# Optimization experiments

Hardware: AMD Instinct MI355X
Metric: run time of the kernel (lower is better)

Reference implementation:

```python
import jax, jax.numpy as jnp
import numpy as np

# Model config (mirrors init_kwargs)
E = 8          # num_experts
K = 2          # top_k
S = 1          # select_top_k
THRESHOLD = 0.7
NORM_TOPK = True
H = 1024       # hidden_dim
F = 1024       # moe intermediate dim
B, SEQ = 2, 1024


def setup_inputs() -> dict:
    key = jax.random.key(0)
    k1, k2, k3, k4, k5 = jax.random.split(key, 5)
    hidden_states = jax.random.normal(k1, (B, SEQ, H), jnp.float32)
    gate_weight = jax.random.normal(k2, (E, H), jnp.float32) * 0.02
    gate_up_proj = jax.random.normal(k3, (E, 2 * F, H), jnp.float32) * 0.02
    down_proj = jax.random.normal(k4, (E, H, F), jnp.float32) * 0.02
    sim = jax.random.uniform(k5, (E, E), jnp.float32)
    sim = (sim + sim.T) / 2.0
    sim = sim.at[jnp.arange(E), jnp.arange(E)].set(1.0)  # fill_diagonal_(1.0)
    return {
        "hidden_states": hidden_states,
        "gate_weight": gate_weight,
        "gate_up_proj": gate_up_proj,
        "down_proj": down_proj,
        "similarity_matrix": sim,
    }


def reference(hidden_states, gate_weight, gate_up_proj, down_proj, similarity_matrix):
    b, s, h = hidden_states.shape
    x = hidden_states.reshape(-1, h)                     # [N, H]
    N = x.shape[0]

    # Router: logits -> softmax(fp32) -> topk (+ optional norm)
    logits = x @ gate_weight.T                           # [N, E]
    probs = jax.nn.softmax(logits.astype(jnp.float32), axis=-1)
    top_w, top_i = jax.lax.top_k(probs, K)               # [N, K]
    if NORM_TOPK:
        top_w = top_w / jnp.clip(jnp.sum(top_w, -1, keepdims=True), 1e-12)

    # SERE reroute: primary = union of top-S experts over batch; map each
    # secondary expert to its most-similar primary if sim >= threshold.
    primary_mask = jnp.zeros((E,), bool).at[top_i[:, :S].reshape(-1)].set(True)
    sim = jnp.where(primary_mask[None, :], similarity_matrix.astype(jnp.float32), -jnp.inf)
    best_j = jnp.argmax(sim, axis=-1)                    # best primary per expert
    best_sim = jnp.max(sim, axis=-1)
    ids = jnp.arange(E)
    expert_map = jnp.where((~primary_mask) & (best_sim >= THRESHOLD), best_j, ids)
    rerouted = expert_map[top_i]                         # [N, K]

    # Merge duplicate slots via scatter-add, then re-topk K.
    rows = jnp.arange(N)[:, None]
    dense = jnp.zeros((N, E), top_w.dtype).at[rows, rerouted].add(top_w)
    fw, fi = jax.lax.top_k(dense, K)                     # nnz per row <= K, so topk keeps all
    combine = jnp.zeros((N, E), fw.dtype).at[rows, fi].add(jnp.where(fw > 0, fw, 0.0))  # [N, E]

    # Expert MLPs (dense jit-friendly dispatch): silu(gate)*up -> down
    gu = jnp.einsum('nh,efh->enf', x, gate_up_proj)      # [E, N, 2F]
    g, u = jnp.split(gu, 2, axis=-1)
    hmid = jax.nn.silu(g) * u                            # [E, N, F]
    y = jnp.einsum('enf,ehf->enh', hmid, down_proj)      # [E, N, H]
    out = jnp.einsum('ne,enh->nh', combine, y)           # weighted combine
    return out.reshape(b, s, h)
```

## Files before the change

kernel.cpp:

```cpp
#include <hip/hip_runtime.h>
#include <cstdint>
#include <cstddef>

#define N_TOK 2048
#define HID 1024
#define FDIM 1024
#define NE 8
#define PAIR_CAP 5120
#define MT 128
#define BK 64
#define THRESH 0.7f

typedef __attribute__((ext_vector_type(8))) short bf16x8;
typedef __attribute__((ext_vector_type(4))) float f32x4;

static __device__ __forceinline__ unsigned short f2bf(float f) {
  unsigned int u = __float_as_uint(f);
  u += 0x7FFF + ((u >> 16) & 1);
  return (unsigned short)(u >> 16);
}

static __device__ __forceinline__ void gl2lds16(const unsigned short* g, unsigned short* l) {
  __builtin_amdgcn_global_load_lds(
      (const __attribute__((address_space(1))) void*)g,
      (__attribute__((address_space(3))) void*)l, 16, 0, 0);
}

__global__ __launch_bounds__(256) void k_router(
    const float* __restrict__ x, const float* __restrict__ gw,
    unsigned short* __restrict__ xb, float* __restrict__ topw,
    int* __restrict__ topi) {
  __shared__ float sgw[NE * HID];
  int t = threadIdx.x;
#pragma unroll
  for (int i = 0; i < NE * HID / 256; ++i) sgw[t + 256 * i] = gw[t + 256 * i];
  __syncthreads();
  int lane = t & 63;
  int wave = t >> 6;
  int n = blockIdx.x * 4 + wave;
  float acc[NE];
#pragma unroll
  for (int e = 0; e < NE; ++e) acc[e] = 0.f;
#pragma unroll
  for (int i = 0; i < HID / 64; ++i) {
    int h = i * 64 + lane;
    float xv = x[(size_t)n * HID + h];
    xb[(size_t)n * HID + h] = f2bf(xv);
#pragma unroll
    for (int e = 0; e < NE; ++e) acc[e] += xv * sgw[e * HID + h];
  }
#pragma unroll
  for (int off = 32; off > 0; off >>= 1) {
#pragma unroll
    for (int e = 0; e < NE; ++e) acc[e] += __shfl_xor(acc[e], off, 64);
  }
  if (lane == 0) {
    float m = acc[0];
    for (int e = 1; e < NE; ++e) m = fmaxf(m, acc[e]);
    float p[NE]; float s = 0.f;
    for (int e = 0; e < NE; ++e) { p[e] = __expf(acc[e] - m); s += p[e]; }
    float inv = 1.f / s;
    for (int e = 0; e < NE; ++e) p[e] *= inv;
    int i0 = 0; float b0 = p[0];
    for (int e = 1; e < NE; ++e) if (p[e] > b0) { b0 = p[e]; i0 = e; }
    int i1 = -1; float b1 = -1.f;
    for (int e = 0; e < NE; ++e) { if (e == i0) continue; if (p[e] > b1) { b1 = p[e]; i1 = e; } }
    float sw = b0 + b1; if (sw < 1e-12f) sw = 1e-12f;
    topw[n * 2] = b0 / sw; topw[n * 2 + 1] = b1 / sw;
    topi[n * 2] = i0;      topi[n * 2 + 1] = i1;
  }
}

__global__ __launch_bounds__(256) void k_pairs(
    const float* __restrict__ sim, const int* __restrict__ topi,
    const float* __restrict__ topw, int* __restrict__ ctrl,
    int* __restrict__ ptok, float* __restrict__ pw) {
  __shared__ int prim[NE], emap[NE], cnt[NE], soff[NE], cur[NE], padc[NE];
  int t = threadIdx.x;
  if (t < NE) { prim[t] = 0; cnt[t] = 0; }
  __syncthreads();
  for (int n = t; n < N_TOK; n += 256) prim[topi[n * 2]] = 1;
  __syncthreads();
  if (t < NE) {
    float best = -1e30f; int bj = -1;
    for (int j = 0; j < NE; ++j) {
      if (prim[j]) {
        float s = sim[t * NE + j];
        if (s > best) { best = s; bj = j; }
      }
    }
    int m = t;
    if (!prim[t] && bj >= 0 && best >= THRESH) m = bj;
    emap[t] = m;
  }
  __syncthreads();
  for (int n = t; n < N_TOK; n += 256) {
    atomicAdd(&cnt[emap[topi[n * 2]]], 1);
    atomicAdd(&cnt[emap[topi[n * 2 + 1]]], 1);
  }
  __syncthreads();
  if (t == 0) {
    int o = 0;
    for (int e = 0; e < NE; ++e) {
      soff[e] = o;
      int p = (cnt[e] + MT - 1) & ~(MT - 1);
      padc[e] = p; cur[e] = 0; o += p;
    }
  }
  __syncthreads();
  if (t < NE) { ctrl[24 + t] = soff[t]; ctrl[32 + t] = padc[t]; }
  for (int n = t; n < N_TOK; n += 256) {
    int i0 = topi[n * 2], i1 = topi[n * 2 + 1];
    int e0 = emap[i0], e1 = emap[i1];
    int s0 = soff[e0] + atomicAdd(&cur[e0], 1);
    int s1 = soff[e1] + atomicAdd(&cur[e1], 1);
    ptok[s0] = n; pw[s0] = topw[n * 2];
    ptok[s1] = n; pw[s1] = topw[n * 2 + 1];
  }
  __syncthreads();
  for (int e = 0; e < NE; ++e) {
    for (int s = cnt[e] + t; s < padc[e]; s += 256) {
      ptok[soff[e] + s] = 0; pw[soff[e] + s] = 0.f;
    }
  }
}


__global__ __launch_bounds__(256, 2) void k_gemm1(
    const unsigned short* __restrict__ xb, const float* __restrict__ gup,
    unsigned short* __restrict__ hmid, const int* __restrict__ ptok,
    const int* __restrict__ ctrl) {
  int b = blockIdx.x;
  int mt = b >> 8;
  int r8 = b & 255;
  int e = r8 >> 5;
  int y = r8 & 31;
  int padc = ctrl[32 + e];
  if (mt * MT >= padc) return;
  int base = ctrl[24 + e] + mt * MT;
  int f0 = y * 32;

  __shared__ unsigned short As[MT * BK];
  __shared__ unsigned short Bs[64 * BK];
  __shared__ int toks[MT];

  int t = threadIdx.x;
  if (t < MT) toks[t] = ptok[base + t];
  __syncthreads();

  int lane = t & 63;
  int wave = t >> 6;
  int wm = wave >> 1, wn = wave & 1;
  int lm = lane & 15, lh = lane >> 4;

  f32x4 acc[4][2] = {};
  const float* gbase = gup + (size_t)e * 2 * FDIM * HID;

  for (int k0 = 0; k0 < HID; k0 += BK) {
    float4 vb[4];
#pragma unroll
    for (int i = 0; i < 4; ++i) {
      int q = i * 256 + t;
      int r = q >> 4, c4 = q & 15;
      vb[i] = *(const float4*)(gbase + (size_t)(((r >> 4) & 1) * FDIM + f0 + ((r >> 5) << 4) + (r & 15)) * HID + k0 + c4 * 4);
    }
#pragma unroll
    for (int i = 0; i < 4; ++i) {
      int q = i * 256 + t;
      int r = q >> 3;
      int cl = (q & 7) ^ (r & 7);
      gl2lds16(xb + (size_t)toks[r] * HID + k0 + cl * 8, &As[(q & ~63) * 8]);
    }
#pragma unroll
    for (int i = 0; i < 4; ++i) {
      int q = i * 256 + t;
      int r = q >> 4, w = q & 15;
      int pch = (w >> 1) ^ (r & 7);
      unsigned long long pk = (unsigned long long)f2bf(vb[i].x)
          | ((unsigned long long)f2bf(vb[i].y) << 16)
          | ((unsigned long long)f2bf(vb[i].z) << 32)
          | ((unsigned long long)f2bf(vb[i].w) << 48);
      *(unsigned long long*)(&Bs[r * BK + pch * 8 + (w & 1) * 4]) = pk;
    }
    __syncthreads();
#pragma unroll
    for (int kk = 0; kk < 2; ++kk) {
      bf16x8 af[4], bfr[2];
#pragma unroll
      for (int rb = 0; rb < 4; ++rb) {
        int row = wm * 64 + rb * 16 + lm;
        int p = (kk * 4 + lh) ^ (row & 7);
        af[rb] = *(const bf16x8*)(&As[row * BK + p * 8]);
      }
#pragma unroll
      for (int cc = 0; cc < 2; ++cc) {
        int row = wn * 32 + cc * 16 + lm;
        int p = (kk * 4 + lh) ^ (row & 7);
        bfr[cc] = *(const bf16x8*)(&Bs[row * BK + p * 8]);
      }
#pragma unroll
      for (int rb = 0; rb < 4; ++rb) {
#pragma unroll
        for (int cc = 0; cc < 2; ++cc)
          acc[rb][cc] = __builtin_amdgcn_mfma_f32_16x16x32_bf16(af[rb], bfr[cc], acc[rb][cc], 0, 0, 0);
      }
    }
    __syncthreads();
  }
#pragma unroll
  for (int rb = 0; rb < 4; ++rb) {
    int slot = base + wm * 64 + rb * 16 + lh * 4;
    f32x4 g = acc[rb][0];
    f32x4 u = acc[rb][1];
    int f = f0 + wn * 16 + lm;
#pragma unroll
    for (int reg = 0; reg < 4; ++reg) {
      float gv = g[reg];
      float hm = gv / (1.f + __expf(-gv)) * u[reg];
      hmid[(size_t)(slot + reg) * FDIM + f] = f2bf(hm);
    }
  }
}

__global__ __launch_bounds__(256, 2) void k_gemm2(
    const unsigned short* __restrict__ hmid, const float* __restrict__ dwn,
    float* __restrict__ out, const int* __restrict__ ptok,
    const float* __restrict__ pw, const int* __restrict__ ctrl) {
  int b = blockIdx.x;
  int mt = b >> 7;
  int r7 = b & 127;
  int e = r7 >> 4;
  int y = r7 & 15;
  int padc = ctrl[32 + e];
  if (mt * MT >= padc) return;
  int base = ctrl[24 + e] + mt * MT;
  int h0 = y * 64;

  __shared__ unsigned short As[MT * BK];
  __shared__ unsigned short Bs[64 * BK];
  __shared__ int stok[MT];
  __shared__ float spw[MT];

  int t = threadIdx.x;
  if (t < MT) { stok[t] = ptok[base + t]; spw[t] = pw[base + t]; }
  __syncthreads();

  int lane = t & 63;
  int wave = t >> 6;
  int wm = wave >> 1, wn = wave & 1;
  int lm = lane & 15, lh = lane >> 4;

  f32x4 acc[4][2] = {};
  const float* dbase = dwn + (size_t)e * HID * FDIM;

  for (int k0 = 0; k0 < FDIM; k0 += BK) {
    float4 vb[4];
#pragma unroll
    for (int i = 0; i < 4; ++i) {
      int q = i * 256 + t;
      int r = q >> 4, c4 = q & 15;
      vb[i] = *(const float4*)(dbase + (size_t)(h0 + r) * FDIM + k0 + c4 * 4);
    }
#pragma unroll
    for (int i = 0; i < 4; ++i) {
      int q = i * 256 + t;
      int r = q >> 3;
      int cl = (q & 7) ^ (r & 7);
      gl2lds16(hmid + (size_t)(base + r) * FDIM + k0 + cl * 8, &As[(q & ~63) * 8]);
    }
#pragma unroll
    for (int i = 0; i < 4; ++i) {
      int q = i * 256 + t;
      int r = q >> 4, w = q & 15;
      int pch = (w >> 1) ^ (r & 7);
      unsigned long long pk = (unsigned long long)f2bf(vb[i].x)
          | ((unsigned long long)f2bf(vb[i].y) << 16)
          | ((unsigned long long)f2bf(vb[i].z) << 32)
          | ((unsigned long long)f2bf(vb[i].w) << 48);
      *(unsigned long long*)(&Bs[r * BK + pch * 8 + (w & 1) * 4]) = pk;
    }
    __syncthreads();
#pragma unroll
    for (int kk = 0; kk < 2; ++kk) {
      bf16x8 af[4], bfr[2];
#pragma unroll
      for (int rb = 0; rb < 4; ++rb) {
        int row = wm * 64 + rb * 16 + lm;
        int p = (kk * 4 + lh) ^ (row & 7);
        af[rb] = *(const bf16x8*)(&As[row * BK + p * 8]);
      }
#pragma unroll
      for (int cc = 0; cc < 2; ++cc) {
        int row = wn * 32 + cc * 16 + lm;
        int p = (kk * 4 + lh) ^ (row & 7);
        bfr[cc] = *(const bf16x8*)(&Bs[row * BK + p * 8]);
      }
#pragma unroll
      for (int rb = 0; rb < 4; ++rb) {
#pragma unroll
        for (int cc = 0; cc < 2; ++cc)
          acc[rb][cc] = __builtin_amdgcn_mfma_f32_16x16x32_bf16(af[rb], bfr[cc], acc[rb][cc], 0, 0, 0);
      }
    }
    __syncthreads();
  }
#pragma unroll
  for (int rb = 0; rb < 4; ++rb) {
    int sl = wm * 64 + rb * 16 + lh * 4;
#pragma unroll
    for (int cc = 0; cc < 2; ++cc) {
      int h = h0 + wn * 32 + cc * 16 + lm;
#pragma unroll
      for (int reg = 0; reg < 4; ++reg) {
        int tok = stok[sl + reg];
        float wgt = spw[sl + reg];
        atomicAdd(&out[(size_t)tok * HID + h], wgt * acc[rb][cc][reg]);
      }
    }
  }
}

extern "C" void kernel_launch(void* const* d_in, const int* in_sizes, int n_in,
                              void* d_out, int out_size, void* d_ws, size_t ws_size,
                              hipStream_t stream) {
  (void)in_sizes; (void)n_in; (void)ws_size;
  const float* x   = (const float*)d_in[0];
  const float* gw  = (const float*)d_in[1];
  const float* gup = (const float*)d_in[2];
  const float* dwn = (const float*)d_in[3];
  const float* sim = (const float*)d_in[4];
  float* out = (float*)d_out;

  char* w = (char*)d_ws;
  int* ctrl = (int*)w;
  size_t off = 256;
  unsigned short* xb = (unsigned short*)(w + off); off += (size_t)N_TOK * HID * 2;
  float* topw = (float*)(w + off); off += (size_t)N_TOK * 2 * 4;
  int*   topi = (int*)(w + off);   off += (size_t)N_TOK * 2 * 4;
  int*   ptok = (int*)(w + off);   off += (size_t)PAIR_CAP * 4;
  float* pw   = (float*)(w + off); off += (size_t)PAIR_CAP * 4;
  unsigned short* hmid = (unsigned short*)(w + off); off += (size_t)PAIR_CAP * FDIM * 2;

  hipMemsetAsync(out, 0, (size_t)out_size * 4, stream);
  k_router<<<N_TOK / 4, 256, 0, stream>>>(x, gw, xb, topw, topi);
  k_pairs<<<1, 256, 0, stream>>>(sim, topi, topw, ctrl, ptok, pw);
  k_gemm1<<<dim3(32 * 256), 256, 0, stream>>>(xb, gup, hmid, ptok, ctrl);
  k_gemm2<<<dim3(32 * 128), 256, 0, stream>>>(hmid, dwn, out, ptok, pw, ctrl);
}
```

Measured before the change: 244.0 us.

## Pre-convert expert weights to bf16 and replace atomic scatter with gather combine

Adds a conversion kernel that turns the fp32 gate_up and down weights into bf16 once per call. Both GEMMs can then stage weights straight into LDS with direct global-to-LDS loads instead of loading fp32 and converting in registers. GEMM2 now writes per-slot bf16 outputs with a narrower tile, and a new combine kernel gathers each token's two slots using the recorded pair positions. This removes the output memset and the fp32 atomics, at the cost of extra weight conversion traffic each call, a yb buffer round trip, and an extra bf16 rounding of the expert outputs.

After: 212.6 us. 1.15x faster.

```diff
diff --git a/kernel.cpp b/kernel.cpp
--- a/kernel.cpp
+++ b/kernel.cpp
@@ -19,11 +19,25 @@
   u += 0x7FFF + ((u >> 16) & 1);
   return (unsigned short)(u >> 16);
 }
+static __device__ __forceinline__ float bf2f(unsigned short u) {
+  return __uint_as_float(((unsigned int)u) << 16);
+}
 
 static __device__ __forceinline__ void gl2lds16(const unsigned short* g, unsigned short* l) {
   __builtin_amdgcn_global_load_lds(
       (const __attribute__((address_space(1))) void*)g,
       (__attribute__((address_space(3))) void*)l, 16, 0, 0);
+}
+
+__global__ __launch_bounds__(256) void k_cvt(
+    const float* __restrict__ src, unsigned short* __restrict__ dst, int n4) {
+  int i = blockIdx.x * 256 + threadIdx.x;
+  if (i < n4) {
+    float4 v = ((const float4*)src)[i];
+    ushort4 o;
+    o.x = f2bf(v.x); o.y = f2bf(v.y); o.z = f2bf(v.z); o.w = f2bf(v.w);
+    ((ushort4*)dst)[i] = o;
+  }
 }
 
 __global__ __launch_bounds__(256) void k_router(
@@ -74,7 +88,7 @@
 __global__ __launch_bounds__(256) void k_pairs(
     const float* __restrict__ sim, const int* __restrict__ topi,
     const float* __restrict__ topw, int* __restrict__ ctrl,
-    int* __restrict__ ptok, float* __restrict__ pw) {
+    int* __restrict__ ptok, float* __restrict__ pw, int* __restrict__ pot) {
   __shared__ int prim[NE], emap[NE], cnt[NE], soff[NE], cur[NE], padc[NE];
   int t = threadIdx.x;
   if (t < NE) { prim[t] = 0; cnt[t] = 0; }
@@ -116,6 +130,7 @@
     int s1 = soff[e1] + atomicAdd(&cur[e1], 1);
     ptok[s0] = n; pw[s0] = topw[n * 2];
     ptok[s1] = n; pw[s1] = topw[n * 2 + 1];
+    pot[n * 2] = s0; pot[n * 2 + 1] = s1;
   }
   __syncthreads();
   for (int e = 0; e < NE; ++e) {
@@ -127,7 +142,7 @@
 
 
 __global__ __launch_bounds__(256, 2) void k_gemm1(
-    const unsigned short* __restrict__ xb, const float* __restrict__ gup,
+    const unsigned short* __restrict__ xb, const unsigned short* __restrict__ gupb,
     unsigned short* __restrict__ hmid, const int* __restrict__ ptok,
     const int* __restrict__ ctrl) {
   int b = blockIdx.x;
@@ -154,16 +169,9 @@
   int lm = lane & 15, lh = lane >> 4;
 
   f32x4 acc[4][2] = {};
-  const float* gbase = gup + (size_t)e * 2 * FDIM * HID;
+  const unsigned short* gbase = gupb + (size_t)e * 2 * FDIM * HID;
 
   for (int k0 = 0; k0 < HID; k0 += BK) {
-    float4 vb[4];
-#pragma unroll
-    for (int i = 0; i < 4; ++i) {
-      int q = i * 256 + t;
-      int r = q >> 4, c4 = q & 15;
-      vb[i] = *(const float4*)(gbase + (size_t)(((r >> 4) & 1) * FDIM + f0 + ((r >> 5) << 4) + (r & 15)) * HID + k0 + c4 * 4);
-    }
 #pragma unroll
     for (int i = 0; i < 4; ++i) {
       int q = i * 256 + t;
@@ -172,15 +180,12 @@
       gl2lds16(xb + (size_t)toks[r] * HID + k0 + cl * 8, &As[(q & ~63) * 8]);
     }
 #pragma unroll
-    for (int i = 0; i < 4; ++i) {
+    for (int i = 0; i < 2; ++i) {
       int q = i * 256 + t;
-      int r = q >> 4, w = q & 15;
-      int pch = (w >> 1) ^ (r & 7);
-      unsigned long long pk = (unsigned long long)f2bf(vb[i].x)
-          | ((unsigned long long)f2bf(vb[i].y) << 16)
-          | ((unsigned long long)f2bf(vb[i].z) << 32)
-          | ((unsigned long long)f2bf(vb[i].w) << 48);
-      *(unsigned long long*)(&Bs[r * BK + pch * 8 + (w & 1) * 4]) = pk;
+      int r = q >> 3;
+      int cl = (q & 7) ^ (r & 7);
+      int grow = ((r >> 4) & 1) * FDIM + f0 + ((r >> 5) << 4) + (r & 15);
+      gl2lds16(gbase + (size_t)grow * HID + k0 + cl * 8, &Bs[(q & ~63) * 8]);
     }
     __syncthreads();
 #pragma unroll
@@ -223,44 +228,31 @@
 }
 
 __global__ __launch_bounds__(256, 2) void k_gemm2(
-    const unsigned short* __restrict__ hmid, const float* __restrict__ dwn,
-    float* __restrict__ out, const int* __restrict__ ptok,
-    const float* __restrict__ pw, const int* __restrict__ ctrl) {
+    const unsigned short* __restrict__ hmid, const unsigned short* __restrict__ dwnb,
+    unsigned short* __restrict__ yb, const int* __restrict__ ctrl) {
   int b = blockIdx.x;
-  int mt = b >> 7;
-  int r7 = b & 127;
-  int e = r7 >> 4;
-  int y = r7 & 15;
+  int mt = b >> 8;
+  int r8 = b & 255;
+  int e = r8 >> 5;
+  int y = r8 & 31;
   int padc = ctrl[32 + e];
   if (mt * MT >= padc) return;
   int base = ctrl[24 + e] + mt * MT;
-  int h0 = y * 64;
+  int h0 = y * 32;
 
   __shared__ unsigned short As[MT * BK];
-  __shared__ unsigned short Bs[64 * BK];
-  __shared__ int stok[MT];
-  __shared__ float spw[MT];
-
-  int t = threadIdx.x;
-  if (t < MT) { stok[t] = ptok[base + t]; spw[t] = pw[base + t]; }
-  __syncthreads();
-
+  __shared__ unsigned short Bs[32 * BK];
+
+  int t = threadIdx.x;
   int lane = t & 63;
   int wave = t >> 6;
   int wm = wave >> 1, wn = wave & 1;
   int lm = lane & 15, lh = lane >> 4;
 
-  f32x4 acc[4][2] = {};
-  const float* dbase = dwn + (size_t)e * HID * FDIM;
+  f32x4 acc[4] = {};
+  const unsigned short* dbase = dwnb + (size_t)e * HID * FDIM;
 
   for (int k0 = 0; k0 < FDIM; k0 += BK) {
-    float4 vb[4];
-#pragma unroll
-    for (int i = 0; i < 4; ++i) {
-      int q = i * 256 + t;
-      int r = q >> 4, c4 = q & 15;
-      vb[i] = *(const float4*)(dbase + (size_t)(h0 + r) * FDIM + k0 + c4 * 4);
-    }
 #pragma unroll
     for (int i = 0; i < 4; ++i) {
       int q = i * 256 + t;
@@ -268,62 +260,65 @@
       int cl = (q & 7) ^ (r & 7);
       gl2lds16(hmid + (size_t)(base + r) * FDIM + k0 + cl * 8, &As[(q & ~63) * 8]);
     }
-#pragma unroll
-    for (int i = 0; i < 4; ++i) {
-      int q = i * 256 + t;
-      int r = q >> 4, w = q & 15;
-      int pch = (w >> 1) ^ (r & 7);
-      unsigned long long pk = (unsigned long long)f2bf(vb[i].x)
-          | ((unsigned long long)f2bf(vb[i].y) << 16)
-          | ((unsigned long long)f2bf(vb[i].z) << 32)
-          | ((unsigned long long)f2bf(vb[i].w) << 48);
-      *(unsigned long long*)(&Bs[r * BK + pch * 8 + (w & 1) * 4]) = pk;
+    {
+      int q = t;
+      int r = q >> 3;
+      int cl = (q & 7) ^ (r & 7);
+      gl2lds16(dbase + (size_t)(h0 + r) * FDIM + k0 + cl * 8, &Bs[(q & ~63) * 8]);
     }
     __syncthreads();
 #pragma unroll
     for (int kk = 0; kk < 2; ++kk) {
-      bf16x8 af[4], bfr[2];
+      bf16x8 af[4], bfr;
 #pragma unroll
       for (int rb = 0; rb < 4; ++rb) {
         int row = wm * 64 + rb * 16 + lm;
         int p = (kk * 4 + lh) ^ (row & 7);
         af[rb] = *(const bf16x8*)(&As[row * BK + p * 8]);
       }
-#pragma unroll
-      for (int cc = 0; cc < 2; ++cc) {
-        int row = wn * 32 + cc * 16 + lm;
+      {
+        int row = wn * 16 + lm;
         int p = (kk * 4 + lh) ^ (row & 7);
-        bfr[cc] = *(const bf16x8*)(&Bs[row * BK + p * 8]);
-      }
-#pragma unroll
-      for (int rb = 0; rb < 4; ++rb) {
-#pragma unroll
-        for (int cc = 0; cc < 2; ++cc)
-          acc[rb][cc] = __builtin_amdgcn_mfma_f32_16x16x32_bf16(af[rb], bfr[cc], acc[rb][cc], 0, 0, 0);
-      }
+        bfr = *(const bf16x8*)(&Bs[row * BK + p * 8]);
+      }
+#pragma unroll
+      for (int rb = 0; rb < 4; ++rb)
+        acc[rb] = __builtin_amdgcn_mfma_f32_16x16x32_bf16(af[rb], bfr, acc[rb], 0, 0, 0);
     }
     __syncthreads();
   }
 #pragma unroll
   for (int rb = 0; rb < 4; ++rb) {
-    int sl = wm * 64 + rb * 16 + lh * 4;
-#pragma unroll
-    for (int cc = 0; cc < 2; ++cc) {
-      int h = h0 + wn * 32 + cc * 16 + lm;
-#pragma unroll
-      for (int reg = 0; reg < 4; ++reg) {
-        int tok = stok[sl + reg];
-        float wgt = spw[sl + reg];
-        atomicAdd(&out[(size_t)tok * HID + h], wgt * acc[rb][cc][reg]);
-      }
-    }
-  }
+    int slot = base + wm * 64 + rb * 16 + lh * 4;
+    int h = h0 + wn * 16 + lm;
+#pragma unroll
+    for (int reg = 0; reg < 4; ++reg)
+      yb[(size_t)(slot + reg) * HID + h] = f2bf(acc[rb][reg]);
+  }
+}
+
+__global__ __launch_bounds__(256) void k_combine(
+    const unsigned short* __restrict__ yb, const float* __restrict__ pw,
+    const int* __restrict__ pot, float* __restrict__ out) {
+  int n = blockIdx.x;
+  int t = threadIdx.x;
+  int p0 = pot[n * 2], p1 = pot[n * 2 + 1];
+  float w0 = pw[p0], w1 = pw[p1];
+  int h = t * 4;
+  ushort4 a = *(const ushort4*)(yb + (size_t)p0 * HID + h);
+  ushort4 b = *(const ushort4*)(yb + (size_t)p1 * HID + h);
+  float4 o;
+  o.x = w0 * bf2f(a.x) + w1 * bf2f(b.x);
+  o.y = w0 * bf2f(a.y) + w1 * bf2f(b.y);
+  o.z = w0 * bf2f(a.z) + w1 * bf2f(b.z);
+  o.w = w0 * bf2f(a.w) + w1 * bf2f(b.w);
+  *(float4*)(out + (size_t)n * HID + h) = o;
 }
 
 extern "C" void kernel_launch(void* const* d_in, const int* in_sizes, int n_in,
                               void* d_out, int out_size, void* d_ws, size_t ws_size,
                               hipStream_t stream) {
-  (void)in_sizes; (void)n_in; (void)ws_size;
+  (void)in_sizes; (void)n_in; (void)out_size; (void)ws_size;
   const float* x   = (const float*)d_in[0];
   const float* gw  = (const float*)d_in[1];
   const float* gup = (const float*)d_in[2];
@@ -339,11 +334,19 @@
   int*   topi = (int*)(w + off);   off += (size_t)N_TOK * 2 * 4;
   int*   ptok = (int*)(w + off);   off += (size_t)PAIR_CAP * 4;
   float* pw   = (float*)(w + off); off += (size_t)PAIR_CAP * 4;
+  int*   pot  = (int*)(w + off);   off += (size_t)N_TOK * 2 * 4;
   unsigned short* hmid = (unsigned short*)(w + off); off += (size_t)PAIR_CAP * FDIM * 2;
-
-  hipMemsetAsync(out, 0, (size_t)out_size * 4, stream);
+  unsigned short* yb   = (unsigned short*)(w + off); off += (size_t)PAIR_CAP * HID * 2;
+  unsigned short* gupb = (unsigned short*)(w + off); off += (size_t)NE * 2 * FDIM * HID * 2;
+  unsigned short* dwnb = (unsigned short*)(w + off); off += (size_t)NE * HID * FDIM * 2;
+
+  int n4g = NE * 2 * FDIM * HID / 4;
+  int n4d = NE * HID * FDIM / 4;
+  k_cvt<<<(n4g + 255) / 256, 256, 0, stream>>>(gup, gupb, n4g);
+  k_cvt<<<(n4d + 255) / 256, 256, 0, stream>>>(dwn, dwnb, n4d);
   k_router<<<N_TOK / 4, 256, 0, stream>>>(x, gw, xb, topw, topi);
-  k_pairs<<<1, 256, 0, stream>>>(sim, topi, topw, ctrl, ptok, pw);
-  k_gemm1<<<dim3(32 * 256), 256, 0, stream>>>(xb, gup, hmid, ptok, ctrl);
-  k_gemm2<<<dim3(32 * 128), 256, 0, stream>>>(hmid, dwn, out, ptok, pw, ctrl);
-}
+  k_pairs<<<1, 256, 0, stream>>>(sim, topi, topw, ctrl, ptok, pw, pot);
+  k_gemm1<<<dim3(32 * 256), 256, 0, stream>>>(xb, gupb, hmid, ptok, ctrl);
+  k_gemm2<<<dim3(32 * 256), 256, 0, stream>>>(hmid, dwnb, yb, ctrl);
+  k_combine<<<N_TOK, 256, 0, stream>>>(yb, pw, pot, out);
+}
```
